# Performance work log

Measured on AMD Instinct MI355X. Metric: run time of the kernel, lower is better.

## Reference

```python
import jax, jax.numpy as jnp
import numpy as np
from math import sqrt

THRESHOLD = 0.5
NEG_POS_RATIO = 3
ALPHA = 1.0


def make_priors():
    fms = [(38, 0.1, [1.0, 2.0, 0.5]), (19, 0.2, [1.0, 2.0, 0.5, 3.0, 1.0 / 3]),
           (10, 0.375, [1.0, 2.0, 0.5, 3.0, 1.0 / 3]), (5, 0.55, [1.0, 2.0, 0.5, 3.0, 1.0 / 3]),
           (3, 0.725, [1.0, 2.0, 0.5]), (1, 0.9, [1.0, 2.0, 0.5])]
    scales = [0.1, 0.2, 0.375, 0.55, 0.725, 0.9]
    priors = []
    for k, (d, s, ratios) in enumerate(fms):
        for i in range(d):
            for j in range(d):
                cx = (i + 0.5) / d
                cy = (j + 0.5) / d
                for r in ratios:
                    priors.append([cx, cy, s * sqrt(r), s / sqrt(r)])
                    if r == 1.0:
                        add = sqrt(scales[k] * scales[k + 1]) if k + 1 < len(scales) else 1.0
                        priors.append([cx, cy, add, add])
    return np.clip(np.asarray(priors, dtype=np.float32), 0.0, 1.0)  # [8732, 4]


def cxcy_to_xy(b):
    return jnp.concatenate([b[..., :2] - b[..., 2:] / 2.0, b[..., :2] + b[..., 2:] / 2.0], -1)


def jaccard(a, b):
    # a: [O,4] cxcy, b: [P,4] cxcy -> IoU [O,P]
    a_xy, b_xy = cxcy_to_xy(a), cxcy_to_xy(b)
    lt = jnp.maximum(a_xy[:, None, :2], b_xy[None, :, :2])
    rb = jnp.minimum(a_xy[:, None, 2:], b_xy[None, :, 2:])
    wh = jnp.clip(rb - lt, 0.0)
    inter = wh[..., 0] * wh[..., 1]
    area_a = (a_xy[:, 2] - a_xy[:, 0]) * (a_xy[:, 3] - a_xy[:, 1])
    area_b = (b_xy[:, 2] - b_xy[:, 0]) * (b_xy[:, 3] - b_xy[:, 1])
    return inter / (area_a[:, None] + area_b[None, :] - inter)


def cxcy_to_gcxgcy(cxcy, priors):
    g_cxcy = (cxcy[..., :2] - priors[..., :2]) / (priors[..., 2:] / 10.0)
    g_wh = jnp.log(cxcy[..., 2:] / priors[..., 2:]) * 5.0
    return jnp.concatenate([g_cxcy, g_wh], -1)


def match_one(boxes_i, priors):
    # boxes_i: [O,4] cxcy
    n_obj = boxes_i.shape[0]
    ov = jaccard(boxes_i, priors)                      # [O, P]
    ov_per_prior = ov.max(0)                           # [P]
    obj_per_prior = ov.argmax(0)                       # [P]
    prior_per_obj = ov.argmax(1)                       # [O]
    obj_per_prior = obj_per_prior.at[prior_per_obj].set(jnp.arange(n_obj))
    ov_per_prior = ov_per_prior.at[prior_per_obj].set(1.0)
    labels = (ov_per_prior >= THRESHOLD).astype(jnp.int32)  # [P], 1=text 0=bg
    true_locs = cxcy_to_gcxgcy(boxes_i[obj_per_prior], priors)  # [P,4]
    return labels, true_locs


def setup_inputs() -> dict:
    key = jax.random.key(0)
    k1, k2, k3, k4 = jax.random.split(key, 4)
    priors = jnp.asarray(make_priors())
    B, P, O = 512, priors.shape[0], 16
    predicted_locs = jax.random.normal(k1, (B, P, 4), dtype=jnp.float32)
    predicted_scores = jax.random.normal(k2, (B, P, 2), dtype=jnp.float32)
    centers = 0.2 + 0.6 * jax.random.uniform(k3, (B, O, 2), dtype=jnp.float32)
    wh = 0.05 + 0.35 * jax.random.uniform(k4, (B, O, 2), dtype=jnp.float32)
    boxes = jnp.concatenate([centers, wh], -1)  # cxcy format
    return {"predicted_locs": predicted_locs, "predicted_scores": predicted_scores,
            "boxes": boxes, "priors": priors}


def reference(predicted_locs, predicted_scores, boxes, priors):
    B, P, _ = predicted_locs.shape
    labels, true_locs = jax.vmap(match_one, in_axes=(0, None))(boxes, priors)  # [B,P], [B,P,4]
    pos = labels != 0
    mask = pos.astype(predicted_locs.dtype)            # [B,P]
    n_pos = pos.sum(1)                                 # [B]

    # localization L1 loss (mean over positive box coordinates)
    loc_abs = jnp.abs(predicted_locs - true_locs).sum(-1)  # [B,P]
    loc_loss = (loc_abs * mask).sum() / (mask.sum() * 4.0)

    # per-prior cross-entropy
    logp = jax.nn.log_softmax(predicted_scores, -1)
    ce = -jnp.take_along_axis(logp, labels[..., None], -1)[..., 0]  # [B,P]

    conf_pos = (ce * mask).sum()
    ce_neg = jnp.where(pos, 0.0, ce)
    ce_neg = jnp.sort(ce_neg, axis=1)[:, ::-1]         # descending
    hard = jnp.arange(P)[None, :] < (NEG_POS_RATIO * n_pos)[:, None]
    conf_hn = (ce_neg * hard.astype(ce_neg.dtype)).sum()
    conf_loss = (conf_pos + conf_hn) / n_pos.sum().astype(predicted_locs.dtype)
    return conf_loss + ALPHA * loc_loss
```

## Files before the change

kernel.cpp:

```cpp
#include <hip/hip_runtime.h>

#define NP 8732
#define NQ (NP / 4)
#define NO 16
#define BLK 256
#define NWAVE (BLK / 64)

__global__ __launch_bounds__(BLK, 2) void mbox_row_kernel(
    const float* __restrict__ plocs,
    const float* __restrict__ pscores,
    const float* __restrict__ boxes,
    const float* __restrict__ priors,
    float* __restrict__ loc_out,
    float* __restrict__ conf_out,
    int*   __restrict__ npos_out)
{
    const int b    = blockIdx.x;
    const int tid  = threadIdx.x;
    const int lane = tid & 63;
    const int wv   = tid >> 6;
    const int par  = tid & 1;
    const int objLo = par << 3;

    __shared__ __align__(16) float s_ce[NP];
    __shared__ unsigned char s_obj[NP];
    __shared__ float s_bcw[NO][4];
    __shared__ float s_bxy[NO][4];
    __shared__ float s_barea[NO];
    __shared__ float s_redv[NO * NWAVE];
    __shared__ int   s_redi[NO * NWAVE];
    __shared__ int   s_bestp[NO];
    __shared__ unsigned int s_hist[16];
    __shared__ float s_tval;
    __shared__ float s_fred[3 * NWAVE];
    __shared__ int   s_ired[NWAVE];

    if (tid < NO * 4) ((float*)s_bcw)[tid] = boxes[(size_t)b * NO * 4 + tid];
    __syncthreads();
    if (tid < NO) {
        float cx = s_bcw[tid][0], cy = s_bcw[tid][1];
        float w  = s_bcw[tid][2], h  = s_bcw[tid][3];
        s_bxy[tid][0] = cx - w * 0.5f; s_bxy[tid][1] = cy - h * 0.5f;
        s_bxy[tid][2] = cx + w * 0.5f; s_bxy[tid][3] = cy + h * 0.5f;
        s_barea[tid] = w * h;
    }
    __syncthreads();

    float rx0[8], ry0[8], rx1[8], ry1[8], ra[8];
#pragma unroll
    for (int j = 0; j < 8; j++) {
        rx0[j] = s_bxy[objLo + j][0]; ry0[j] = s_bxy[objLo + j][1];
        rx1[j] = s_bxy[objLo + j][2]; ry1[j] = s_bxy[objLo + j][3];
        ra[j]  = s_barea[objLo + j];
    }

    float tbv[8]; int tbp[8];
#pragma unroll
    for (int j = 0; j < 8; j++) { tbv[j] = -1.0f; tbp[j] = 0; }

    for (int p = (tid >> 1); p < NP; p += (BLK / 2)) {
        float4 pr = ((const float4*)priors)[p];
        float px0 = pr.x - pr.z * 0.5f, py0 = pr.y - pr.w * 0.5f;
        float px1 = pr.x + pr.z * 0.5f, py1 = pr.y + pr.w * 0.5f;
        float areab = pr.z * pr.w;
        float bv = -1.0f; int bo = objLo;
#pragma unroll
        for (int j = 0; j < 8; j++) {
            float ix0 = fmaxf(rx0[j], px0);
            float iy0 = fmaxf(ry0[j], py0);
            float ix1 = fminf(rx1[j], px1);
            float iy1 = fminf(ry1[j], py1);
            float iw = fmaxf(ix1 - ix0, 0.0f);
            float ih = fmaxf(iy1 - iy0, 0.0f);
            float inter = iw * ih;
            float den = ra[j] + areab - inter;
            float iou = inter * __builtin_amdgcn_rcpf(den);
            if (iou > bv)     { bv = iou; bo = objLo + j; }
            if (iou > tbv[j]) { tbv[j] = iou; tbp[j] = p; }
        }
        float vN = __shfl_xor(bv, 1, 64);
        int   oN = __shfl_xor(bo, 1, 64);
        bool take = par ? (vN >= bv) : (vN > bv);
        if (take) { bv = vN; bo = oN; }
        if (par == 0) {
            bool pos = (bv >= 0.5f);
            s_obj[p] = (unsigned char)(bo | (pos ? 0x80 : 0));
        }
    }

#pragma unroll
    for (int j = 0; j < 8; j++) {
        float v = tbv[j]; int i = tbp[j];
        for (int off = 32; off >= 2; off >>= 1) {
            float v2 = __shfl_down(v, off, 64);
            int   i2 = __shfl_down(i, off, 64);
            if (v2 > v || (v2 == v && i2 < i)) { v = v2; i = i2; }
        }
        if (lane < 2) {
            s_redv[(objLo + j) * NWAVE + wv] = v;
            s_redi[(objLo + j) * NWAVE + wv] = i;
        }
    }
    __syncthreads();
    if (tid < NO) {
        float v = s_redv[tid * NWAVE]; int i = s_redi[tid * NWAVE];
#pragma unroll
        for (int w = 1; w < NWAVE; w++) {
            float v2 = s_redv[tid * NWAVE + w]; int i2 = s_redi[tid * NWAVE + w];
            if (v2 > v || (v2 == v && i2 < i)) { v = v2; i = i2; }
        }
        s_bestp[tid] = i;
    }
    __syncthreads();
    if (tid == 0) {
#pragma unroll
        for (int o = 0; o < NO; o++) s_obj[s_bestp[o]] = (unsigned char)(0x80 | o);
    }
    __syncthreads();

    float loc_sum = 0.0f, conf_pos = 0.0f; int np = 0;
    const float2* sc2 = (const float2*)(pscores + (size_t)b * NP * 2);
    const float4* pl4 = (const float4*)(plocs  + (size_t)b * NP * 4);
    for (int p = tid; p < NP; p += BLK) {
        unsigned m = s_obj[p];
        bool pos = (m & 0x80) != 0;
        float2 s = sc2[p];
        float mx = fmaxf(s.x, s.y);
        float dd = fabsf(s.x - s.y);
        float lse = mx + __logf(1.0f + __expf(-dd));
        float ce = lse - (pos ? s.y : s.x);
        if (pos) {
            np++;
            conf_pos += ce;
            int o = m & 15;
            float4 pr = ((const float4*)priors)[p];
            float gx = (s_bcw[o][0] - pr.x) / (pr.z / 10.0f);
            float gy = (s_bcw[o][1] - pr.y) / (pr.w / 10.0f);
            float gw = __logf(s_bcw[o][2] / pr.z) * 5.0f;
            float gh = __logf(s_bcw[o][3] / pr.w) * 5.0f;
            float4 pl = pl4[p];
            loc_sum += fabsf(pl.x - gx) + fabsf(pl.y - gy)
                     + fabsf(pl.z - gw) + fabsf(pl.w - gh);
            s_ce[p] = 0.0f;
        } else {
            s_ce[p] = ce;
        }
    }

    int npw = np;
    for (int off = 32; off; off >>= 1) npw += __shfl_down(npw, off, 64);
    if (lane == 0) s_ired[wv] = npw;
    __syncthreads();
    int n_pos = 0;
#pragma unroll
    for (int w = 0; w < NWAVE; w++) n_pos += s_ired[w];

    const int K = 3 * n_pos;
    const bool selAll = (K >= NP);
    float t = 0.0f;
    const float4* ce4 = (const float4*)s_ce;
    if (!selAll) {
        unsigned prefix = 0u, kk = (unsigned)K;
        bool done = false;
        for (int shift = 28; shift >= 0 && !done; shift -= 4) {
            __syncthreads();
            if (tid < 16) s_hist[tid] = 0u;
            __syncthreads();
            unsigned maskhi = (shift == 28) ? 0u : (0xFFFFFFFFu << (shift + 4));
            for (int q = tid; q < NQ; q += BLK) {
                float4 v = ce4[q];
#pragma unroll
                for (int j = 0; j < 4; j++) {
                    unsigned u = __float_as_uint(j == 0 ? v.x : j == 1 ? v.y : j == 2 ? v.z : v.w);
                    if ((u & maskhi) == prefix)
                        atomicAdd(&s_hist[(u >> shift) & 15u], 1u);
                }
            }
            __syncthreads();
            int dsel = 15; unsigned cnt;
            for (;; dsel--) {
                cnt = s_hist[dsel];
                if (kk <= cnt || dsel == 0) break;
                kk -= cnt;
            }
            prefix |= ((unsigned)dsel << shift);
            if (shift > 0 && cnt == 1u) {
                unsigned mh = 0xFFFFFFFFu << shift;
                for (int q = tid; q < NQ; q += BLK) {
                    float4 v = ce4[q];
#pragma unroll
                    for (int j = 0; j < 4; j++) {
                        float f = (j == 0 ? v.x : j == 1 ? v.y : j == 2 ? v.z : v.w);
                        if ((__float_as_uint(f) & mh) == prefix) s_tval = f;
                    }
                }
                __syncthreads();
                t = s_tval;
                done = true;
            } else if (shift == 0) {
                t = __uint_as_float(prefix);
            }
        }
    }

    float sgt = 0.0f; int cgt = 0;
    for (int q = tid; q < NQ; q += BLK) {
        float4 v = ce4[q];
        if (selAll || v.x > t) { sgt += v.x; cgt++; }
        if (selAll || v.y > t) { sgt += v.y; cgt++; }
        if (selAll || v.z > t) { sgt += v.z; cgt++; }
        if (selAll || v.w > t) { sgt += v.w; cgt++; }
    }

    float a = sgt, c = conf_pos, l = loc_sum; int g = cgt;
    for (int off = 32; off; off >>= 1) {
        a += __shfl_down(a, off, 64);
        c += __shfl_down(c, off, 64);
        l += __shfl_down(l, off, 64);
        g += __shfl_down(g, off, 64);
    }
    __syncthreads();
    if (lane == 0) {
        s_fred[wv] = a; s_fred[NWAVE + wv] = c; s_fred[2 * NWAVE + wv] = l;
        s_ired[wv] = g;
    }
    __syncthreads();
    if (tid == 0) {
        float sa = 0.0f, sc = 0.0f, sl = 0.0f; int sg = 0;
#pragma unroll
        for (int w = 0; w < NWAVE; w++) {
            sa += s_fred[w]; sc += s_fred[NWAVE + w]; sl += s_fred[2 * NWAVE + w];
            sg += s_ired[w];
        }
        float conf_hn = selAll ? sa : (sa + (float)(K - sg) * t);
        conf_out[b] = sc + conf_hn;
        loc_out[b]  = sl;
        npos_out[b] = n_pos;
    }
}

__global__ __launch_bounds__(256) void mbox_finalize_kernel(
    const float* __restrict__ loc_in,
    const float* __restrict__ conf_in,
    const int*   __restrict__ npos_in,
    int B, float* __restrict__ out)
{
    __shared__ float sl[4], sc[4];
    __shared__ int   si[4];
    int tid = threadIdx.x, lane = tid & 63, wv = tid >> 6;
    float l = 0.0f, c = 0.0f; int n = 0;
    for (int i = tid; i < B; i += 256) { l += loc_in[i]; c += conf_in[i]; n += npos_in[i]; }
    for (int off = 32; off; off >>= 1) {
        l += __shfl_down(l, off, 64);
        c += __shfl_down(c, off, 64);
        n += __shfl_down(n, off, 64);
    }
    if (lane == 0) { sl[wv] = l; sc[wv] = c; si[wv] = n; }
    __syncthreads();
    if (tid == 0) {
        float tl = sl[0] + sl[1] + sl[2] + sl[3];
        float tc = sc[0] + sc[1] + sc[2] + sc[3];
        int   tn = si[0] + si[1] + si[2] + si[3];
        float fn = (float)tn;
        out[0] = tc / fn + tl / (fn * 4.0f);
    }
}

extern "C" void kernel_launch(void* const* d_in, const int* in_sizes, int n_in,
                              void* d_out, int out_size, void* d_ws, size_t ws_size,
                              hipStream_t stream) {
    const float* plocs   = (const float*)d_in[0];
    const float* pscores = (const float*)d_in[1];
    const float* boxes   = (const float*)d_in[2];
    const float* priors  = (const float*)d_in[3];
    const int B = in_sizes[0] / (NP * 4);

    float* loc_ws  = (float*)d_ws;
    float* conf_ws = loc_ws + B;
    int*   np_ws   = (int*)(conf_ws + B);

    mbox_row_kernel<<<B, BLK, 0, stream>>>(plocs, pscores, boxes, priors,
                                           loc_ws, conf_ws, np_ws);
    mbox_finalize_kernel<<<1, 256, 0, stream>>>(loc_ws, conf_ws, np_ws, B, (float*)d_out);
}
```

Before: 214.2 us.

## Split prior matching into its own multi-block kernel and use 3-pass radix select

Prior-to-object matching moves into a separate kernel launched over a (batch, SPLIT=4) grid, with each block handling a quarter of the priors. It writes per-prior match bytes and per-chunk best-prior candidates to workspace, and a second loss kernel merges them. The hard-negative threshold search changes from up to eight 4-bit radix passes to three passes with 4096/4096/128-bucket histograms and a block-wide prefix-scan selection. This adds more parallelism when the batch is small, at the cost of an extra launch, a global round trip for the match data, and larger shared-memory histograms that may reduce occupancy. The old fused kernel stays as a fallback when the workspace is too small.

```diff
diff --git a/kernel.cpp b/kernel.cpp
--- a/kernel.cpp
+++ b/kernel.cpp
@@ -5,41 +5,34 @@
 #define NO 16
 #define BLK 256
 #define NWAVE (BLK / 64)
-
-__global__ __launch_bounds__(BLK, 2) void mbox_row_kernel(
-    const float* __restrict__ plocs,
-    const float* __restrict__ pscores,
+#define SPLIT 4
+#define CHUNK (NP / SPLIT)
+
+
+__global__ __launch_bounds__(BLK, 2) void match_kernel(
     const float* __restrict__ boxes,
     const float* __restrict__ priors,
-    float* __restrict__ loc_out,
-    float* __restrict__ conf_out,
-    int*   __restrict__ npos_out)
+    unsigned char* __restrict__ g_obj,
+    float* __restrict__ g_bv,
+    int*   __restrict__ g_bi)
 {
     const int b    = blockIdx.x;
+    const int s    = blockIdx.y;
     const int tid  = threadIdx.x;
     const int lane = tid & 63;
     const int wv   = tid >> 6;
     const int par  = tid & 1;
     const int objLo = par << 3;
-
-    __shared__ __align__(16) float s_ce[NP];
-    __shared__ unsigned char s_obj[NP];
-    __shared__ float s_bcw[NO][4];
+    const int lo = s * CHUNK, hi = lo + CHUNK;
+
     __shared__ float s_bxy[NO][4];
     __shared__ float s_barea[NO];
     __shared__ float s_redv[NO * NWAVE];
     __shared__ int   s_redi[NO * NWAVE];
-    __shared__ int   s_bestp[NO];
-    __shared__ unsigned int s_hist[16];
-    __shared__ float s_tval;
-    __shared__ float s_fred[3 * NWAVE];
-    __shared__ int   s_ired[NWAVE];
-
-    if (tid < NO * 4) ((float*)s_bcw)[tid] = boxes[(size_t)b * NO * 4 + tid];
-    __syncthreads();
+
     if (tid < NO) {
-        float cx = s_bcw[tid][0], cy = s_bcw[tid][1];
-        float w  = s_bcw[tid][2], h  = s_bcw[tid][3];
+        const float* bx = boxes + (size_t)b * NO * 4 + tid * 4;
+        float cx = bx[0], cy = bx[1], w = bx[2], h = bx[3];
         s_bxy[tid][0] = cx - w * 0.5f; s_bxy[tid][1] = cy - h * 0.5f;
         s_bxy[tid][2] = cx + w * 0.5f; s_bxy[tid][3] = cy + h * 0.5f;
         s_barea[tid] = w * h;
@@ -56,9 +49,10 @@
 
     float tbv[8]; int tbp[8];
 #pragma unroll
-    for (int j = 0; j < 8; j++) { tbv[j] = -1.0f; tbp[j] = 0; }
-
-    for (int p = (tid >> 1); p < NP; p += (BLK / 2)) {
+    for (int j = 0; j < 8; j++) { tbv[j] = -1.0f; tbp[j] = lo; }
+
+    unsigned char* obj_row = g_obj + (size_t)b * NP;
+    for (int p = lo + (tid >> 1); p < hi; p += (BLK / 2)) {
         float4 pr = ((const float4*)priors)[p];
         float px0 = pr.x - pr.z * 0.5f, py0 = pr.y - pr.w * 0.5f;
         float px1 = pr.x + pr.z * 0.5f, py1 = pr.y + pr.w * 0.5f;
@@ -84,7 +78,7 @@
         if (take) { bv = vN; bo = oN; }
         if (par == 0) {
             bool pos = (bv >= 0.5f);
-            s_obj[p] = (unsigned char)(bo | (pos ? 0x80 : 0));
+            obj_row[p] = (unsigned char)(bo | (pos ? 0x80 : 0));
         }
     }
 
@@ -107,6 +101,91 @@
 #pragma unroll
         for (int w = 1; w < NWAVE; w++) {
             float v2 = s_redv[tid * NWAVE + w]; int i2 = s_redi[tid * NWAVE + w];
+            if (v2 > v || (v2 == v && i2 < i)) { v = v2; i = i2; }
+        }
+        g_bv[((size_t)b * NO + tid) * SPLIT + s] = v;
+        g_bi[((size_t)b * NO + tid) * SPLIT + s] = i;
+    }
+}
+
+__device__ __forceinline__ int hist_select(unsigned* hist, unsigned* s_part,
+                                           unsigned* s_csuf, unsigned* s_sel,
+                                           unsigned& kk, int tid, int lane, int wv)
+{
+    unsigned ps = 0;
+#pragma unroll
+    for (int i = 0; i < 16; i++) ps += hist[tid * 16 + i];
+    s_part[tid] = ps;
+    __syncthreads();
+    if (wv == 0) {
+        unsigned c0 = s_part[4 * lane + 0], c1 = s_part[4 * lane + 1];
+        unsigned c2 = s_part[4 * lane + 2], c3 = s_part[4 * lane + 3];
+        unsigned g = c0 + c1 + c2 + c3;
+        unsigned incl = g;
+#pragma unroll
+        for (int off = 1; off < 64; off <<= 1) {
+            unsigned o = __shfl_down(incl, off, 64);
+            if (lane + off < 64) incl += o;
+        }
+        unsigned excl = incl - g;
+        s_csuf[4 * lane + 3] = excl;
+        s_csuf[4 * lane + 2] = excl + c3;
+        s_csuf[4 * lane + 1] = excl + c3 + c2;
+        s_csuf[4 * lane + 0] = excl + c3 + c2 + c1;
+    }
+    __syncthreads();
+    unsigned base = s_csuf[tid];
+    if (base < kk && kk <= base + s_part[tid]) {
+        unsigned run = base;
+        for (int i = 15; i >= 0; i--) {
+            unsigned h = hist[tid * 16 + i];
+            if (kk <= run + h) { s_sel[0] = (unsigned)(tid * 16 + i); s_sel[1] = kk - run; break; }
+            run += h;
+        }
+    }
+    __syncthreads();
+    kk = s_sel[1];
+    return (int)s_sel[0];
+}
+
+__global__ __launch_bounds__(BLK, 2) void loss_kernel(
+    const float* __restrict__ plocs,
+    const float* __restrict__ pscores,
+    const float* __restrict__ boxes,
+    const float* __restrict__ priors,
+    const unsigned char* __restrict__ g_obj,
+    const float* __restrict__ g_bv,
+    const int*   __restrict__ g_bi,
+    float* __restrict__ loc_out,
+    float* __restrict__ conf_out,
+    int*   __restrict__ npos_out)
+{
+    const int b    = blockIdx.x;
+    const int tid  = threadIdx.x;
+    const int lane = tid & 63;
+    const int wv   = tid >> 6;
+
+    __shared__ __align__(16) float s_ce[NP];
+    __shared__ unsigned char s_obj[NP];
+    __shared__ unsigned s_hist[4096];
+    __shared__ unsigned s_part[256];
+    __shared__ unsigned s_csuf[256];
+    __shared__ unsigned s_sel[2];
+    __shared__ float s_bcw[NO][4];
+    __shared__ int   s_bestp[NO];
+    __shared__ float s_fred[3 * NWAVE];
+    __shared__ int   s_ired[NWAVE];
+
+    const unsigned char* obj_row = g_obj + (size_t)b * NP;
+    for (int p = tid; p < NP; p += BLK) s_obj[p] = obj_row[p];
+    if (tid < NO * 4) ((float*)s_bcw)[tid] = boxes[(size_t)b * NO * 4 + tid];
+    if (tid < NO) {
+        const float* bv = g_bv + ((size_t)b * NO + tid) * SPLIT;
+        const int*   bi = g_bi + ((size_t)b * NO + tid) * SPLIT;
+        float v = bv[0]; int i = bi[0];
+#pragma unroll
+        for (int s = 1; s < SPLIT; s++) {
+            float v2 = bv[s]; int i2 = bi[s];
             if (v2 > v || (v2 == v && i2 < i)) { v = v2; i = i2; }
         }
         s_bestp[tid] = i;
@@ -160,47 +239,44 @@
     float t = 0.0f;
     const float4* ce4 = (const float4*)s_ce;
     if (!selAll) {
-        unsigned prefix = 0u, kk = (unsigned)K;
-        bool done = false;
-        for (int shift = 28; shift >= 0 && !done; shift -= 4) {
-            __syncthreads();
-            if (tid < 16) s_hist[tid] = 0u;
-            __syncthreads();
-            unsigned maskhi = (shift == 28) ? 0u : (0xFFFFFFFFu << (shift + 4));
-            for (int q = tid; q < NQ; q += BLK) {
-                float4 v = ce4[q];
-#pragma unroll
-                for (int j = 0; j < 4; j++) {
-                    unsigned u = __float_as_uint(j == 0 ? v.x : j == 1 ? v.y : j == 2 ? v.z : v.w);
-                    if ((u & maskhi) == prefix)
-                        atomicAdd(&s_hist[(u >> shift) & 15u], 1u);
-                }
+        unsigned kk = (unsigned)K;
+        for (int i = tid; i < 4096; i += BLK) s_hist[i] = 0u;
+        __syncthreads();
+        for (int q = tid; q < NQ; q += BLK) {
+            float4 v = ce4[q];
+            atomicAdd(&s_hist[__float_as_uint(v.x) >> 19], 1u);
+            atomicAdd(&s_hist[__float_as_uint(v.y) >> 19], 1u);
+            atomicAdd(&s_hist[__float_as_uint(v.z) >> 19], 1u);
+            atomicAdd(&s_hist[__float_as_uint(v.w) >> 19], 1u);
+        }
+        __syncthreads();
+        unsigned b1 = (unsigned)hist_select(s_hist, s_part, s_csuf, s_sel, kk, tid, lane, wv);
+        for (int i = tid; i < 4096; i += BLK) s_hist[i] = 0u;
+        __syncthreads();
+        for (int q = tid; q < NQ; q += BLK) {
+            float4 v = ce4[q];
+#pragma unroll
+            for (int j = 0; j < 4; j++) {
+                unsigned u = __float_as_uint(j == 0 ? v.x : j == 1 ? v.y : j == 2 ? v.z : v.w);
+                if ((u >> 19) == b1) atomicAdd(&s_hist[(u >> 7) & 0xFFFu], 1u);
             }
-            __syncthreads();
-            int dsel = 15; unsigned cnt;
-            for (;; dsel--) {
-                cnt = s_hist[dsel];
-                if (kk <= cnt || dsel == 0) break;
-                kk -= cnt;
+        }
+        __syncthreads();
+        unsigned b2 = (unsigned)hist_select(s_hist, s_part, s_csuf, s_sel, kk, tid, lane, wv);
+        unsigned p2 = (b1 << 12) | b2;
+        for (int i = tid; i < 4096; i += BLK) s_hist[i] = 0u;
+        __syncthreads();
+        for (int q = tid; q < NQ; q += BLK) {
+            float4 v = ce4[q];
+#pragma unroll
+            for (int j = 0; j < 4; j++) {
+                unsigned u = __float_as_uint(j == 0 ? v.x : j == 1 ? v.y : j == 2 ? v.z : v.w);
+                if ((u >> 7) == p2) atomicAdd(&s_hist[u & 0x7Fu], 1u);
             }
-            prefix |= ((unsigned)dsel << shift);
-            if (shift > 0 && cnt == 1u) {
-                unsigned mh = 0xFFFFFFFFu << shift;
-                for (int q = tid; q < NQ; q += BLK) {
-                    float4 v = ce4[q];
-#pragma unroll
-                    for (int j = 0; j < 4; j++) {
-                        float f = (j == 0 ? v.x : j == 1 ? v.y : j == 2 ? v.z : v.w);
-                        if ((__float_as_uint(f) & mh) == prefix) s_tval = f;
-                    }
-                }
-                __syncthreads();
-                t = s_tval;
-                done = true;
-            } else if (shift == 0) {
-                t = __uint_as_float(prefix);
-            }
-        }
+        }
+        __syncthreads();
+        unsigned b3 = (unsigned)hist_select(s_hist, s_part, s_csuf, s_sel, kk, tid, lane, wv);
+        t = __uint_as_float((p2 << 7) | b3);
     }
 
     float sgt = 0.0f; int cgt = 0;
@@ -239,14 +315,184 @@
     }
 }
 
+__global__ __launch_bounds__(BLK, 2) void mbox_row_kernel(
+    const float* __restrict__ plocs, const float* __restrict__ pscores,
+    const float* __restrict__ boxes, const float* __restrict__ priors,
+    float* __restrict__ loc_out, float* __restrict__ conf_out,
+    int* __restrict__ npos_out)
+{
+    const int b = blockIdx.x, tid = threadIdx.x, lane = tid & 63, wv = tid >> 6;
+    const int par = tid & 1, objLo = par << 3;
+    __shared__ __align__(16) float s_ce[NP];
+    __shared__ unsigned char s_obj[NP];
+    __shared__ float s_bcw[NO][4], s_bxy[NO][4], s_barea[NO];
+    __shared__ float s_redv[NO * NWAVE]; __shared__ int s_redi[NO * NWAVE];
+    __shared__ int s_bestp[NO];
+    __shared__ unsigned s_hist16[16];
+    __shared__ float s_tval;
+    __shared__ float s_fred[3 * NWAVE]; __shared__ int s_ired[NWAVE];
+
+    if (tid < NO * 4) ((float*)s_bcw)[tid] = boxes[(size_t)b * NO * 4 + tid];
+    __syncthreads();
+    if (tid < NO) {
+        float cx = s_bcw[tid][0], cy = s_bcw[tid][1], w = s_bcw[tid][2], h = s_bcw[tid][3];
+        s_bxy[tid][0] = cx - w * 0.5f; s_bxy[tid][1] = cy - h * 0.5f;
+        s_bxy[tid][2] = cx + w * 0.5f; s_bxy[tid][3] = cy + h * 0.5f;
+        s_barea[tid] = w * h;
+    }
+    __syncthreads();
+    float rx0[8], ry0[8], rx1[8], ry1[8], ra[8];
+#pragma unroll
+    for (int j = 0; j < 8; j++) {
+        rx0[j] = s_bxy[objLo + j][0]; ry0[j] = s_bxy[objLo + j][1];
+        rx1[j] = s_bxy[objLo + j][2]; ry1[j] = s_bxy[objLo + j][3];
+        ra[j]  = s_barea[objLo + j];
+    }
+    float tbv[8]; int tbp[8];
+#pragma unroll
+    for (int j = 0; j < 8; j++) { tbv[j] = -1.0f; tbp[j] = 0; }
+    for (int p = (tid >> 1); p < NP; p += (BLK / 2)) {
+        float4 pr = ((const float4*)priors)[p];
+        float px0 = pr.x - pr.z * 0.5f, py0 = pr.y - pr.w * 0.5f;
+        float px1 = pr.x + pr.z * 0.5f, py1 = pr.y + pr.w * 0.5f;
+        float areab = pr.z * pr.w;
+        float bv = -1.0f; int bo = objLo;
+#pragma unroll
+        for (int j = 0; j < 8; j++) {
+            float ix0 = fmaxf(rx0[j], px0), iy0 = fmaxf(ry0[j], py0);
+            float ix1 = fminf(rx1[j], px1), iy1 = fminf(ry1[j], py1);
+            float iw = fmaxf(ix1 - ix0, 0.0f), ih = fmaxf(iy1 - iy0, 0.0f);
+            float inter = iw * ih, den = ra[j] + areab - inter;
+            float iou = inter * __builtin_amdgcn_rcpf(den);
+            if (iou > bv) { bv = iou; bo = objLo + j; }
+            if (iou > tbv[j]) { tbv[j] = iou; tbp[j] = p; }
+        }
+        float vN = __shfl_xor(bv, 1, 64); int oN = __shfl_xor(bo, 1, 64);
+        bool take = par ? (vN >= bv) : (vN > bv);
+        if (take) { bv = vN; bo = oN; }
+        if (par == 0) s_obj[p] = (unsigned char)(bo | ((bv >= 0.5f) ? 0x80 : 0));
+    }
+#pragma unroll
+    for (int j = 0; j < 8; j++) {
+        float v = tbv[j]; int i = tbp[j];
+        for (int off = 32; off >= 2; off >>= 1) {
+            float v2 = __shfl_down(v, off, 64); int i2 = __shfl_down(i, off, 64);
+            if (v2 > v || (v2 == v && i2 < i)) { v = v2; i = i2; }
+        }
+        if (lane < 2) { s_redv[(objLo + j) * NWAVE + wv] = v; s_redi[(objLo + j) * NWAVE + wv] = i; }
+    }
+    __syncthreads();
+    if (tid < NO) {
+        float v = s_redv[tid * NWAVE]; int i = s_redi[tid * NWAVE];
+#pragma unroll
+        for (int w = 1; w < NWAVE; w++) {
+            float v2 = s_redv[tid * NWAVE + w]; int i2 = s_redi[tid * NWAVE + w];
+            if (v2 > v || (v2 == v && i2 < i)) { v = v2; i = i2; }
+        }
+        s_bestp[tid] = i;
+    }
+    __syncthreads();
+    if (tid == 0) {
+#pragma unroll
+        for (int o = 0; o < NO; o++) s_obj[s_bestp[o]] = (unsigned char)(0x80 | o);
+    }
+    __syncthreads();
+    float loc_sum = 0.0f, conf_pos = 0.0f; int np = 0;
+    const float2* sc2 = (const float2*)(pscores + (size_t)b * NP * 2);
+    const float4* pl4 = (const float4*)(plocs + (size_t)b * NP * 4);
+    for (int p = tid; p < NP; p += BLK) {
+        unsigned m = s_obj[p]; bool pos = (m & 0x80) != 0;
+        float2 s = sc2[p];
+        float mx = fmaxf(s.x, s.y), dd = fabsf(s.x - s.y);
+        float ce = mx + __logf(1.0f + __expf(-dd)) - (pos ? s.y : s.x);
+        if (pos) {
+            np++; conf_pos += ce;
+            int o = m & 15;
+            float4 pr = ((const float4*)priors)[p];
+            float gx = (s_bcw[o][0] - pr.x) / (pr.z / 10.0f);
+            float gy = (s_bcw[o][1] - pr.y) / (pr.w / 10.0f);
+            float gw = __logf(s_bcw[o][2] / pr.z) * 5.0f;
+            float gh = __logf(s_bcw[o][3] / pr.w) * 5.0f;
+            float4 pl = pl4[p];
+            loc_sum += fabsf(pl.x - gx) + fabsf(pl.y - gy) + fabsf(pl.z - gw) + fabsf(pl.w - gh);
+            s_ce[p] = 0.0f;
+        } else s_ce[p] = ce;
+    }
+    int npw = np;
+    for (int off = 32; off; off >>= 1) npw += __shfl_down(npw, off, 64);
+    if (lane == 0) s_ired[wv] = npw;
+    __syncthreads();
+    int n_pos = 0;
+#pragma unroll
+    for (int w = 0; w < NWAVE; w++) n_pos += s_ired[w];
+    const int K = 3 * n_pos; const bool selAll = (K >= NP);
+    float t = 0.0f;
+    const float4* ce4 = (const float4*)s_ce;
+    if (!selAll) {
+        unsigned prefix = 0u, kk = (unsigned)K; bool done = false;
+        for (int shift = 28; shift >= 0 && !done; shift -= 4) {
+            __syncthreads();
+            if (tid < 16) s_hist16[tid] = 0u;
+            __syncthreads();
+            unsigned maskhi = (shift == 28) ? 0u : (0xFFFFFFFFu << (shift + 4));
+            for (int q = tid; q < NQ; q += BLK) {
+                float4 v = ce4[q];
+#pragma unroll
+                for (int j = 0; j < 4; j++) {
+                    unsigned u = __float_as_uint(j == 0 ? v.x : j == 1 ? v.y : j == 2 ? v.z : v.w);
+                    if ((u & maskhi) == prefix) atomicAdd(&s_hist16[(u >> shift) & 15u], 1u);
+                }
+            }
+            __syncthreads();
+            int dsel = 15; unsigned cnt;
+            for (;; dsel--) { cnt = s_hist16[dsel]; if (kk <= cnt || dsel == 0) break; kk -= cnt; }
+            prefix |= ((unsigned)dsel << shift);
+            if (shift > 0 && cnt == 1u) {
+                unsigned mh = 0xFFFFFFFFu << shift;
+                for (int q = tid; q < NQ; q += BLK) {
+                    float4 v = ce4[q];
+#pragma unroll
+                    for (int j = 0; j < 4; j++) {
+                        float f = (j == 0 ? v.x : j == 1 ? v.y : j == 2 ? v.z : v.w);
+                        if ((__float_as_uint(f) & mh) == prefix) s_tval = f;
+                    }
+                }
+                __syncthreads();
+                t = s_tval; done = true;
+            } else if (shift == 0) t = __uint_as_float(prefix);
+        }
+    }
+    float sgt = 0.0f; int cgt = 0;
+    for (int q = tid; q < NQ; q += BLK) {
+        float4 v = ce4[q];
+        if (selAll || v.x > t) { sgt += v.x; cgt++; }
+        if (selAll || v.y > t) { sgt += v.y; cgt++; }
+        if (selAll || v.z > t) { sgt += v.z; cgt++; }
+        if (selAll || v.w > t) { sgt += v.w; cgt++; }
+    }
+    float a = sgt, c = conf_pos, l = loc_sum; int g = cgt;
+    for (int off = 32; off; off >>= 1) {
+        a += __shfl_down(a, off, 64); c += __shfl_down(c, off, 64);
+        l += __shfl_down(l, off, 64); g += __shfl_down(g, off, 64);
+    }
+    __syncthreads();
+    if (lane == 0) { s_fred[wv] = a; s_fred[NWAVE + wv] = c; s_fred[2 * NWAVE + wv] = l; s_ired[wv] = g; }
+    __syncthreads();
+    if (tid == 0) {
+        float sa = 0, sc = 0, sl = 0; int sg = 0;
+#pragma unroll
+        for (int w = 0; w < NWAVE; w++) { sa += s_fred[w]; sc += s_fred[NWAVE + w]; sl += s_fred[2 * NWAVE + w]; sg += s_ired[w]; }
+        float conf_hn = selAll ? sa : (sa + (float)(K - sg) * t);
+        conf_out[b] = sc + conf_hn; loc_out[b] = sl; npos_out[b] = n_pos;
+    }
+}
+
 __global__ __launch_bounds__(256) void mbox_finalize_kernel(
-    const float* __restrict__ loc_in,
-    const float* __restrict__ conf_in,
-    const int*   __restrict__ npos_in,
-    int B, float* __restrict__ out)
+    const float* __restrict__ loc_in, const float* __restrict__ conf_in,
+    const int* __restrict__ npos_in, int B, float* __restrict__ out)
 {
     __shared__ float sl[4], sc[4];
-    __shared__ int   si[4];
+    __shared__ int si[4];
     int tid = threadIdx.x, lane = tid & 63, wv = tid >> 6;
     float l = 0.0f, c = 0.0f; int n = 0;
     for (int i = tid; i < B; i += 256) { l += loc_in[i]; c += conf_in[i]; n += npos_in[i]; }
@@ -260,7 +506,7 @@
     if (tid == 0) {
         float tl = sl[0] + sl[1] + sl[2] + sl[3];
         float tc = sc[0] + sc[1] + sc[2] + sc[3];
-        int   tn = si[0] + si[1] + si[2] + si[3];
+        int tn = si[0] + si[1] + si[2] + si[3];
         float fn = (float)tn;
         out[0] = tc / fn + tl / (fn * 4.0f);
     }
@@ -278,8 +524,18 @@
     float* loc_ws  = (float*)d_ws;
     float* conf_ws = loc_ws + B;
     int*   np_ws   = (int*)(conf_ws + B);
-
-    mbox_row_kernel<<<B, BLK, 0, stream>>>(plocs, pscores, boxes, priors,
-                                           loc_ws, conf_ws, np_ws);
+    float* g_bv    = (float*)(np_ws + B);
+    int*   g_bi    = (int*)(g_bv + (size_t)B * NO * SPLIT);
+    unsigned char* g_obj = (unsigned char*)(g_bi + (size_t)B * NO * SPLIT);
+    size_t need = (size_t)(3 * B) * 4 + (size_t)B * NO * SPLIT * 8 + (size_t)B * NP;
+
+    if (ws_size >= need) {
+        match_kernel<<<dim3(B, SPLIT), BLK, 0, stream>>>(boxes, priors, g_obj, g_bv, g_bi);
+        loss_kernel<<<B, BLK, 0, stream>>>(plocs, pscores, boxes, priors,
+                                           g_obj, g_bv, g_bi, loc_ws, conf_ws, np_ws);
+    } else {
+        mbox_row_kernel<<<B, BLK, 0, stream>>>(plocs, pscores, boxes, priors,
+                                               loc_ws, conf_ws, np_ws);
+    }
     mbox_finalize_kernel<<<1, 256, 0, stream>>>(loc_ws, conf_ws, np_ws, B, (float*)d_out);
 }
```

Measured after the change: 201.0 us. 6.2% less time.
